# Kernel tuning notes

Hardware: AMD Instinct MI355X
Metric: run time of the kernel (lower is better)

## Reference

```python
import jax, jax.numpy as jnp
import numpy as np

N_NODES = 100000
N_EDGES = 1600000
F_IN, F_HID, F_OUT = 15, 64, 64
N_MID = 6  # layers 1..6 of 8


def gcn_norm(edge_index, edge_weight, num_nodes):
    """PyG GCNConv normalization with self-loops (fill_value=1.0).
    Returns (src, dst, norm) over the augmented edge set."""
    src, dst = edge_index[0], edge_index[1]
    loop = jnp.arange(num_nodes)
    s = jnp.concatenate([src, loop])
    d = jnp.concatenate([dst, loop])
    w = jnp.concatenate([edge_weight, jnp.ones((num_nodes,), edge_weight.dtype)])
    deg = jax.ops.segment_sum(w, d, num_segments=num_nodes)
    dinv = jnp.where(deg > 0, jax.lax.rsqrt(deg), 0.0)
    norm = dinv[s] * w * dinv[d]  # [E+N]
    return s, d, norm


def gcn_layer(h, s, d, norm, W, b, num_nodes):
    h = h @ W                                  # dense transform [N, F_out]
    msg = norm[:, None] * h[s]                 # gather + scale   [E+N, F_out]
    out = jax.ops.segment_sum(msg, d, num_segments=num_nodes)  # scatter-add
    return out + b


def setup_inputs() -> dict:
    key = jax.random.key(0)
    ks = jax.random.split(key, 8)
    x = jax.random.normal(ks[0], (N_NODES, F_IN), jnp.float32)
    edge_index = jax.random.randint(ks[1], (2, N_EDGES), 0, N_NODES, jnp.int64)
    edge_weight = jax.random.uniform(ks[2], (N_EDGES,), jnp.float32)
    # glorot-ish scaling keeps activations sane through 8 layers
    W0 = jax.random.normal(ks[3], (F_IN, F_HID), jnp.float32) * (1.0 / np.sqrt(F_IN))
    b0 = jnp.zeros((F_HID,), jnp.float32)
    W_mid = jax.random.normal(ks[4], (N_MID, F_HID, F_HID), jnp.float32) * (1.0 / np.sqrt(F_HID))
    b_mid = jnp.zeros((N_MID, F_HID), jnp.float32)
    W_last = jax.random.normal(ks[5], (F_HID, F_OUT), jnp.float32) * (1.0 / np.sqrt(F_HID))
    b_last = jnp.zeros((F_OUT,), jnp.float32)
    return {"x": x, "edge_index": edge_index, "edge_weight": edge_weight,
            "W0": W0, "b0": b0, "W_mid": W_mid, "b_mid": b_mid,
            "W_last": W_last, "b_last": b_last}


def reference(x, edge_index, edge_weight, W0, b0, W_mid, b_mid, W_last, b_last):
    num_nodes = x.shape[0]
    s, d, norm = gcn_norm(edge_index, edge_weight, num_nodes)
    # layer 0
    h = gcn_layer(x, s, d, norm, W0, b0, num_nodes)
    h = jax.nn.relu(h)  # dropout is identity in eval mode
    # middle layers 1..6
    for i in range(N_MID):
        h = gcn_layer(h, s, d, norm, W_mid[i], b_mid[i], num_nodes)
        h = jax.nn.relu(h)
    # final layer + sigmoid
    h = gcn_layer(h, s, d, norm, W_last, b_last, num_nodes)
    return jax.nn.sigmoid(h)
```

## Files before the change

kernel.cpp:

```cpp
#include <hip/hip_runtime.h>
#include <hip/hip_fp16.h>
#include <math.h>

#define N_NODES 100000
#define N_EDGES 1600000
#define F_IN 15
#define MASK40 ((1ull << 40) - 1)

#define NBLK1 256
#define EPB   (N_EDGES / NBLK1)
#define NBUCK 256
#define NBUCK_USED ((N_NODES + 511) >> 9)

typedef _Float16 half8 __attribute__((ext_vector_type(8)));
typedef float f32x4 __attribute__((ext_vector_type(4)));


__global__ __launch_bounds__(1024) void k_hist(const int* __restrict__ dst,
                                               int* __restrict__ hist) {
    __shared__ int bins[NBUCK];
    int t = threadIdx.x, blk = blockIdx.x;
    if (t < NBUCK) bins[t] = 0;
    __syncthreads();
    int e0 = blk * EPB;
    for (int e = e0 + t; e < e0 + EPB; e += 1024)
        atomicAdd(&bins[dst[e] >> 9], 1);
    __syncthreads();
    if (t < NBUCK) hist[t * NBLK1 + blk] = bins[t];
}

__global__ __launch_bounds__(1024) void k_scan(int* __restrict__ hist,
                                               int* __restrict__ bucketBase,
                                               int* __restrict__ rowptr) {
    __shared__ int sc[1024];
    int t = threadIdx.x;
    int base = t * 64;
    int vals[64];
    int tot = 0;
#pragma unroll
    for (int k = 0; k < 64; k++) { vals[k] = hist[base + k]; tot += vals[k]; }
    sc[t] = tot;
    __syncthreads();
    for (int off = 1; off < 1024; off <<= 1) {
        int u = (t >= off) ? sc[t - off] : 0;
        __syncthreads();
        sc[t] += u;
        __syncthreads();
    }
    int run = sc[t] - tot;
#pragma unroll
    for (int k = 0; k < 64; k++) {
        int idx = base + k;
        if ((idx & (NBLK1 - 1)) == 0) bucketBase[idx / NBLK1] = run;
        int v = vals[k];
        hist[idx] = run;
        run += v;
    }
    if (t == 0) { bucketBase[NBUCK] = N_EDGES; rowptr[N_NODES] = N_EDGES; }
}

__global__ __launch_bounds__(1024) void k_scatter(const int* __restrict__ src,
        const int* __restrict__ dst, const float* __restrict__ w,
        const int* __restrict__ hist, int2* __restrict__ brec) {
    __shared__ int cursor[NBUCK];
    int t = threadIdx.x, blk = blockIdx.x;
    if (t < NBUCK) cursor[t] = hist[t * NBLK1 + blk];
    __syncthreads();
    int e0 = blk * EPB;
    for (int e = e0 + t; e < e0 + EPB; e += 1024) {
        int d = dst[e];
        int pos = atomicAdd(&cursor[d >> 9], 1);
        brec[pos] = make_int2(src[e] | ((d & 511) << 17), __float_as_int(w[e]));
    }
}

__global__ __launch_bounds__(512) void k_deg(const int2* __restrict__ brec,
        const int* __restrict__ bucketBase, float* __restrict__ dinv,
        int* __restrict__ rowptr) {
    __shared__ unsigned long long packedl[512];
    __shared__ int sc[512];
    int t = threadIdx.x, b = blockIdx.x;
    packedl[t] = 0ull;
    __syncthreads();
    int ebase = bucketBase[b], eend = bucketBase[b + 1];
    for (int e = ebase + t; e < eend; e += 512) {
        int2 r = brec[e];
        int dlo = (r.x >> 17) & 511;
        float wv = __int_as_float(r.y);
        unsigned long long contrib =
            (1ull << 40) + (unsigned long long)((double)wv * 4294967296.0);
        atomicAdd(&packedl[dlo], contrib);
    }
    __syncthreads();
    unsigned long long p = packedl[t];
    int cnt = (int)(p >> 40);
    int n = (b << 9) + t;
    if (n < N_NODES) {
        float deg = 1.0f + (float)((double)(p & MASK40) * 0x1p-32);
        dinv[n] = rsqrtf(deg);
    }
    sc[t] = cnt;
    __syncthreads();
    for (int off = 1; off < 512; off <<= 1) {
        int u = (t >= off) ? sc[t - off] : 0;
        __syncthreads();
        sc[t] += u;
        __syncthreads();
    }
    if (n < N_NODES) rowptr[n] = ebase + sc[t] - cnt;
}

__global__ __launch_bounds__(512) void k_csr(const int2* __restrict__ brec,
        const int* __restrict__ bucketBase, const int* __restrict__ rowptr,
        const float* __restrict__ dinv, int2* __restrict__ csr) {
    __shared__ int cursor[512];
    __shared__ float dl[512];
    int t = threadIdx.x, b = blockIdx.x;
    int n = (b << 9) + t;
    if (n < N_NODES) { cursor[t] = rowptr[n]; dl[t] = dinv[n]; }
    else             { cursor[t] = 0;         dl[t] = 0.f; }
    __syncthreads();
    int ebase = bucketBase[b], eend = bucketBase[b + 1];
    for (int e = ebase + t; e < eend; e += 512) {
        int2 r = brec[e];
        int dlo = (r.x >> 17) & 511;
        int s = r.x & 0x1FFFF;
        float wv = __int_as_float(r.y);
        int slot = atomicAdd(&cursor[dlo], 1);
        float nm = dinv[s] * wv * dl[dlo];
        csr[slot] = make_int2(s, __float_as_int(nm));
    }
}


__global__ void k_gemm0(const float* __restrict__ x, const float* __restrict__ W,
                        __half* __restrict__ out) {
    __shared__ float Ws[F_IN * 64];
    int t = threadIdx.x;
    for (int i = t; i < F_IN * 64; i += 256) Ws[i] = W[i];
    __syncthreads();
    int r = blockIdx.x * 4 + (t >> 6);
    int c = t & 63;
    if (r < N_NODES) {
        const float* xr = x + (long)r * F_IN;
        float acc = 0.f;
#pragma unroll
        for (int k = 0; k < F_IN; k++) acc += xr[k] * Ws[k * 64 + c];
        out[(long)r * 64 + c] = __float2half(acc);
    }
}


#define SE_CAP 256
#define G_STRIDE 72

template <bool WEP, bool SIG>
__global__ __launch_bounds__(256) void k_gather4(
        const int* __restrict__ rowptr, const int2* __restrict__ csr,
        const __half* __restrict__ hin, const float* __restrict__ dinv,
        const float* __restrict__ W, const float* __restrict__ b,
        void* __restrict__ outp) {
    extern __shared__ char smem[];
    int t = threadIdx.x, wv = t >> 6, lane = t & 63;
    int sub = lane >> 5, fl = lane & 31;
    int2* se = (int2*)smem + wv * SE_CAP;
    _Float16* G = (_Float16*)(smem + 4 * SE_CAP * 8);

    int nb = blockIdx.x * 32;
    int n0w = nb + wv * 8;

    int rp[9];
#pragma unroll
    for (int j = 0; j < 9; j++) rp[j] = rowptr[n0w + j];
    int base = rp[0], end = rp[8];

    const __half2* h2 = (const __half2*)hin;

    float2 acc[8];
#pragma unroll
    for (int j = 0; j < 8; j++) {
        int n = n0w + j;
        float dv = dinv[n];
        float2 hf = __half22float2(h2[(long)n * 32 + fl]);
        float w0 = (sub == 0) ? dv * dv : 0.f;
        acc[j].x = w0 * hf.x;
        acc[j].y = w0 * hf.y;
    }

    for (int cb = base; cb < end; cb += SE_CAP) {
        int ce = cb + SE_CAP; if (ce > end) ce = end;
        int cn = ce - cb;
        for (int i = lane; i < cn; i += 64) se[i] = csr[cb + i];
        __builtin_amdgcn_wave_barrier();
#pragma unroll
        for (int j = 0; j < 8; j++) {
            int lo = rp[j] < cb ? cb : rp[j];
            int hi = rp[j + 1] > ce ? ce : rp[j + 1];
            int i = lo - cb, iend = hi - cb;
            for (; i + 7 < iend; i += 8) {
                int2 r0 = se[i + sub],     r1 = se[i + 2 + sub];
                int2 r2 = se[i + 4 + sub], r3 = se[i + 6 + sub];
                float2 f0 = __half22float2(h2[(long)r0.x * 32 + fl]);
                float2 f1 = __half22float2(h2[(long)r1.x * 32 + fl]);
                float2 f2 = __half22float2(h2[(long)r2.x * 32 + fl]);
                float2 f3 = __half22float2(h2[(long)r3.x * 32 + fl]);
                float n0 = __int_as_float(r0.y), n1 = __int_as_float(r1.y);
                float n2 = __int_as_float(r2.y), n3 = __int_as_float(r3.y);
                acc[j].x += n0 * f0.x; acc[j].y += n0 * f0.y;
                acc[j].x += n1 * f1.x; acc[j].y += n1 * f1.y;
                acc[j].x += n2 * f2.x; acc[j].y += n2 * f2.y;
                acc[j].x += n3 * f3.x; acc[j].y += n3 * f3.y;
            }
            for (; i + 1 < iend; i += 2) {
                int2 r = se[i + sub];
                float2 f = __half22float2(h2[(long)r.x * 32 + fl]);
                float nm = __int_as_float(r.y);
                acc[j].x += nm * f.x; acc[j].y += nm * f.y;
            }
            if (i < iend) {
                int2 r = se[i];
                float2 f = __half22float2(h2[(long)r.x * 32 + fl]);
                float nm = (sub == 0) ? __int_as_float(r.y) : 0.f;
                acc[j].x += nm * f.x; acc[j].y += nm * f.y;
            }
        }
        __builtin_amdgcn_wave_barrier();
    }

#pragma unroll
    for (int j = 0; j < 8; j++) {
        acc[j].x += __shfl_xor(acc[j].x, 32);
        acc[j].y += __shfl_xor(acc[j].y, 32);
    }

    if (!WEP) {
        float2 bv = ((const float2*)b)[fl];
        if (sub == 0) {
#pragma unroll
            for (int j = 0; j < 8; j++) {
                float ox = fmaxf(acc[j].x + bv.x, 0.f);
                float oy = fmaxf(acc[j].y + bv.y, 0.f);
                ((__half2*)outp)[(long)(n0w + j) * 32 + fl] = __floats2half2_rn(ox, oy);
            }
        }
        return;
    }

    if (sub == 0) {
        __half2* G2 = (__half2*)G;
#pragma unroll
        for (int j = 0; j < 8; j++)
            G2[(wv * 8 + j) * (G_STRIDE / 2) + fl] = __floats2half2_rn(acc[j].x, acc[j].y);
    }
    __syncthreads();

    int col = lane & 15, quad = lane >> 4;
    int mrow = (wv & 1) * 16;
    int nc0 = (wv >> 1) * 32;

    half8 af[2];
#pragma unroll
    for (int kt = 0; kt < 2; kt++)
        af[kt] = *(const half8*)&G[(mrow + col) * G_STRIDE + kt * 32 + quad * 8];

    half8 bf[2][2][2];
#pragma unroll
    for (int nt = 0; nt < 2; nt++) {
#pragma unroll
        for (int kt = 0; kt < 2; kt++) {
#pragma unroll
            for (int j = 0; j < 8; j++) {
                float w = W[(kt * 32 + quad * 8 + j) * 64 + nc0 + nt * 16 + col];
                _Float16 hi = (_Float16)w;
                bf[nt][kt][0][j] = hi;
                bf[nt][kt][1][j] = (_Float16)(w - (float)hi);
            }
        }
    }

    f32x4 c0, c1;
    {
        float b0v = b[nc0 + col], b1v = b[nc0 + 16 + col];
        c0 = (f32x4){b0v, b0v, b0v, b0v};
        c1 = (f32x4){b1v, b1v, b1v, b1v};
    }
#pragma unroll
    for (int kt = 0; kt < 2; kt++) {
        c0 = __builtin_amdgcn_mfma_f32_16x16x32_f16(af[kt], bf[0][kt][0], c0, 0, 0, 0);
        c0 = __builtin_amdgcn_mfma_f32_16x16x32_f16(af[kt], bf[0][kt][1], c0, 0, 0, 0);
        c1 = __builtin_amdgcn_mfma_f32_16x16x32_f16(af[kt], bf[1][kt][0], c1, 0, 0, 0);
        c1 = __builtin_amdgcn_mfma_f32_16x16x32_f16(af[kt], bf[1][kt][1], c1, 0, 0, 0);
    }

#pragma unroll
    for (int nt = 0; nt < 2; nt++) {
        f32x4 c = nt ? c1 : c0;
#pragma unroll
        for (int r = 0; r < 4; r++) {
            long node = nb + mrow + quad * 4 + r;
            int feat = nc0 + nt * 16 + col;
            float o = c[r];
            if (SIG) {
                o = 1.0f / (1.0f + expf(-o));
                ((float*)outp)[node * 64 + feat] = o;
            } else {
                o = fmaxf(o, 0.f);
                ((__half*)outp)[node * 64 + feat] = __float2half(o);
            }
        }
    }
}


extern "C" void kernel_launch(void* const* d_in, const int* in_sizes, int n_in,
                              void* d_out, int out_size, void* d_ws, size_t ws_size,
                              hipStream_t stream) {
    const float* x  = (const float*)d_in[0];
    const int*   ei = (const int*)  d_in[1];
    const float* ew = (const float*)d_in[2];
    const float* W0 = (const float*)d_in[3];
    const float* b0 = (const float*)d_in[4];
    const float* Wm = (const float*)d_in[5];
    const float* bm = (const float*)d_in[6];
    const float* Wl = (const float*)d_in[7];
    const float* bl = (const float*)d_in[8];
    float* out = (float*)d_out;

    const int* src = ei;
    const int* dst = ei + N_EDGES;

    char* ws = (char*)d_ws;
    int*    hist   = (int*)  (ws + 0);
    int*    bbase  = (int*)  (ws + (1u << 18));
    float*  dinv   = (float*)(ws + (1u << 20));
    int*    rowptr = (int*)  (ws + (2u << 20));
    int2*   brec   = (int2*) (ws + (3u << 20));
    int2*   csr    = (int2*) (ws + (16u << 20));
    __half* htmp   = (__half*)(ws + (29u << 20));
    __half* hA     = (__half*)(ws + (42u << 20));
    __half* hB     = (__half*)(ws + (55u << 20));

    int gR4 = (N_NODES + 3) / 4;
    int gG  = N_NODES / 32;

    const size_t smem0 = 4 * SE_CAP * 8;
    const size_t smemW = 4 * SE_CAP * 8 + 32 * G_STRIDE * 2;

    hipLaunchKernelGGL(k_hist,    dim3(NBLK1), dim3(1024), 0, stream, dst, hist);
    hipLaunchKernelGGL(k_scan,    dim3(1),     dim3(1024), 0, stream, hist, bbase, rowptr);
    hipLaunchKernelGGL(k_scatter, dim3(NBLK1), dim3(1024), 0, stream, src, dst, ew, hist, brec);
    hipLaunchKernelGGL(k_deg,     dim3(NBUCK_USED), dim3(512), 0, stream, brec, bbase, dinv, rowptr);
    hipLaunchKernelGGL(k_csr,     dim3(NBUCK_USED), dim3(512), 0, stream, brec, bbase, rowptr, dinv, csr);

    hipLaunchKernelGGL(k_gemm0,   dim3(gR4), dim3(256), 0, stream, x, W0, htmp);
    hipLaunchKernelGGL((k_gather4<false, false>), dim3(gG), dim3(256), smem0, stream,
                       rowptr, csr, htmp, dinv, (const float*)nullptr, b0, (void*)hA);

    __half* hin = hA;
    __half* hout = hB;
    for (int i = 0; i < 6; i++) {
        const float* Wi = Wm + (long)i * 64 * 64;
        const float* bi = bm + (long)i * 64;
        hipLaunchKernelGGL((k_gather4<true, false>), dim3(gG), dim3(256), smemW, stream,
                           rowptr, csr, hin, dinv, Wi, bi, (void*)hout);
        __half* t2 = hin; hin = hout; hout = t2;
    }

    hipLaunchKernelGGL((k_gather4<true, true>), dim3(gG), dim3(256), smemW, stream,
                       rowptr, csr, hin, dinv, Wl, bl, (void*)out);
}
```

Measured before the change: 505.6 us.

## Stage gather-kernel outputs through LDS for vectorized stores, shrink edge cache

The fused gather+MFMA kernel now writes its 32x64 result tile into shared memory and then emits 16-byte vector stores (half8 for hidden layers, float4 for the sigmoid output), where it previously used scattered 2/4-byte stores. SE_CAP is halved and launch bounds request 8 blocks per CU, which shrinks LDS and register use so more blocks can be resident. The accumulation is rewritten with explicit fmaf and half-to-float extraction. The extra barriers and the LDS round trip add some latency, and the float staging with stride 66 may be misaligned for float4 reads.

After: 509.8 us. No clear change (+0.8%).

```diff
diff --git a/kernel.cpp b/kernel.cpp
--- a/kernel.cpp
+++ b/kernel.cpp
@@ -151,11 +151,11 @@
 }
 
 
-#define SE_CAP 256
+#define SE_CAP 128
 #define G_STRIDE 72
 
 template <bool WEP, bool SIG>
-__global__ __launch_bounds__(256) void k_gather4(
+__global__ __launch_bounds__(256, 8) void k_gather4(
         const int* __restrict__ rowptr, const int2* __restrict__ csr,
         const __half* __restrict__ hin, const float* __restrict__ dinv,
         const float* __restrict__ W, const float* __restrict__ b,
@@ -181,10 +181,10 @@
     for (int j = 0; j < 8; j++) {
         int n = n0w + j;
         float dv = dinv[n];
-        float2 hf = __half22float2(h2[(long)n * 32 + fl]);
+        __half2 hq = h2[(long)n * 32 + fl];
         float w0 = (sub == 0) ? dv * dv : 0.f;
-        acc[j].x = w0 * hf.x;
-        acc[j].y = w0 * hf.y;
+        acc[j].x = w0 * __low2float(hq);
+        acc[j].y = w0 * __high2float(hq);
     }
 
     for (int cb = base; cb < end; cb += SE_CAP) {
@@ -200,28 +200,34 @@
             for (; i + 7 < iend; i += 8) {
                 int2 r0 = se[i + sub],     r1 = se[i + 2 + sub];
                 int2 r2 = se[i + 4 + sub], r3 = se[i + 6 + sub];
-                float2 f0 = __half22float2(h2[(long)r0.x * 32 + fl]);
-                float2 f1 = __half22float2(h2[(long)r1.x * 32 + fl]);
-                float2 f2 = __half22float2(h2[(long)r2.x * 32 + fl]);
-                float2 f3 = __half22float2(h2[(long)r3.x * 32 + fl]);
+                __half2 q0 = h2[(long)r0.x * 32 + fl];
+                __half2 q1 = h2[(long)r1.x * 32 + fl];
+                __half2 q2 = h2[(long)r2.x * 32 + fl];
+                __half2 q3 = h2[(long)r3.x * 32 + fl];
                 float n0 = __int_as_float(r0.y), n1 = __int_as_float(r1.y);
                 float n2 = __int_as_float(r2.y), n3 = __int_as_float(r3.y);
-                acc[j].x += n0 * f0.x; acc[j].y += n0 * f0.y;
-                acc[j].x += n1 * f1.x; acc[j].y += n1 * f1.y;
-                acc[j].x += n2 * f2.x; acc[j].y += n2 * f2.y;
-                acc[j].x += n3 * f3.x; acc[j].y += n3 * f3.y;
+                acc[j].x = fmaf(n0, __low2float(q0), acc[j].x);
+                acc[j].y = fmaf(n0, __high2float(q0), acc[j].y);
+                acc[j].x = fmaf(n1, __low2float(q1), acc[j].x);
+                acc[j].y = fmaf(n1, __high2float(q1), acc[j].y);
+                acc[j].x = fmaf(n2, __low2float(q2), acc[j].x);
+                acc[j].y = fmaf(n2, __high2float(q2), acc[j].y);
+                acc[j].x = fmaf(n3, __low2float(q3), acc[j].x);
+                acc[j].y = fmaf(n3, __high2float(q3), acc[j].y);
             }
             for (; i + 1 < iend; i += 2) {
                 int2 r = se[i + sub];
-                float2 f = __half22float2(h2[(long)r.x * 32 + fl]);
+                __half2 q = h2[(long)r.x * 32 + fl];
                 float nm = __int_as_float(r.y);
-                acc[j].x += nm * f.x; acc[j].y += nm * f.y;
+                acc[j].x = fmaf(nm, __low2float(q), acc[j].x);
+                acc[j].y = fmaf(nm, __high2float(q), acc[j].y);
             }
             if (i < iend) {
                 int2 r = se[i];
-                float2 f = __half22float2(h2[(long)r.x * 32 + fl]);
+                __half2 q = h2[(long)r.x * 32 + fl];
                 float nm = (sub == 0) ? __int_as_float(r.y) : 0.f;
-                acc[j].x += nm * f.x; acc[j].y += nm * f.y;
+                acc[j].x = fmaf(nm, __low2float(q), acc[j].x);
+                acc[j].y = fmaf(nm, __high2float(q), acc[j].y);
             }
         }
         __builtin_amdgcn_wave_barrier();
@@ -262,6 +268,8 @@
 #pragma unroll
     for (int kt = 0; kt < 2; kt++)
         af[kt] = *(const half8*)&G[(mrow + col) * G_STRIDE + kt * 32 + quad * 8];
+
+    __syncthreads();
 
     half8 bf[2][2][2];
 #pragma unroll
@@ -292,21 +300,41 @@
         c1 = __builtin_amdgcn_mfma_f32_16x16x32_f16(af[kt], bf[1][kt][1], c1, 0, 0, 0);
     }
 
-#pragma unroll
-    for (int nt = 0; nt < 2; nt++) {
-        f32x4 c = nt ? c1 : c0;
-#pragma unroll
-        for (int r = 0; r < 4; r++) {
-            long node = nb + mrow + quad * 4 + r;
-            int feat = nc0 + nt * 16 + col;
-            float o = c[r];
-            if (SIG) {
-                o = 1.0f / (1.0f + expf(-o));
-                ((float*)outp)[node * 64 + feat] = o;
-            } else {
-                o = fmaxf(o, 0.f);
-                ((__half*)outp)[node * 64 + feat] = __float2half(o);
-            }
+    if (!SIG) {
+#pragma unroll
+        for (int nt = 0; nt < 2; nt++) {
+            f32x4 c = nt ? c1 : c0;
+#pragma unroll
+            for (int r = 0; r < 4; r++) {
+                float o = fmaxf(c[r], 0.f);
+                G[(mrow + quad * 4 + r) * G_STRIDE + nc0 + nt * 16 + col] =
+                    (_Float16)o;
+            }
+        }
+        __syncthreads();
+        {
+            int row = t >> 3, seg = t & 7;
+            half8 v = *(const half8*)&G[row * G_STRIDE + seg * 8];
+            *(half8*)((__half*)outp + (long)(nb + row) * 64 + seg * 8) = v;
+        }
+    } else {
+        float* fo = (float*)smem;
+#pragma unroll
+        for (int nt = 0; nt < 2; nt++) {
+            f32x4 c = nt ? c1 : c0;
+#pragma unroll
+            for (int r = 0; r < 4; r++) {
+                float o = 1.0f / (1.0f + expf(-c[r]));
+                fo[(mrow + quad * 4 + r) * 66 + nc0 + nt * 16 + col] = o;
+            }
+        }
+        __syncthreads();
+#pragma unroll
+        for (int k = 0; k < 2; k++) {
+            int lin = t + k * 256;
+            int row = lin >> 4, seg = lin & 15;
+            float4 v = *(const float4*)&fo[row * 66 + seg * 4];
+            *(float4*)((float*)outp + (long)(nb + row) * 64 + seg * 4) = v;
         }
     }
 }
```
